# Kernel optimization log

Hardware: AMD Instinct MI355X
Metric: run time of the kernel (lower is better)

## Reference

```python
import jax, jax.numpy as jnp
import numpy as np

N_NODES = 100000
N_EDGES = 300000
D = 256
N_LAYERS = 4
BN_EPS = 1e-5


def setup_inputs() -> dict:
    key = jax.random.key(0)
    ks = jax.random.split(key, 6)
    x = jax.random.normal(ks[0], (N_NODES, D), dtype=jnp.float32)
    rows = jax.random.randint(ks[1], (N_EDGES,), 0, N_NODES)
    cols = jax.random.randint(ks[2], (N_EDGES,), 0, N_NODES)
    vals = jax.random.uniform(ks[3], (N_EDGES,), dtype=jnp.float32)
    stdv = 1.0 / np.sqrt(D).astype(np.float32)
    weights = jax.random.uniform(ks[4], (N_LAYERS, D, D), jnp.float32, -stdv, stdv)
    self_weights = jax.random.uniform(ks[5], (N_LAYERS, D, D), jnp.float32, -stdv, stdv)
    gammas = jnp.ones((N_LAYERS, D), jnp.float32)
    betas = jnp.zeros((N_LAYERS, D), jnp.float32)
    return {"x": x, "vals": vals, "weights": weights, "self_weights": self_weights,
            "gammas": gammas, "betas": betas, "rows": rows, "cols": cols}


def reference(x, vals, weights, self_weights, gammas, betas, rows, cols):
    n = x.shape[0]

    def gcn_layer(h, W, SW, gamma, beta):
        # support = h @ W  -> dense [N, D]
        support = h @ W
        # spmm(adj, support): out[i] = sum_{e: rows[e]==i} vals[e] * support[cols[e]]
        agg = jax.ops.segment_sum(vals[:, None] * support[cols], rows, num_segments=n)
        out = agg + h @ SW  # self-loop term (withloop=True)
        # BatchNorm1d over nodes (training-mode batch stats, biased variance)
        mean = out.mean(axis=0)
        var = out.var(axis=0)
        out = gamma * (out - mean) * jax.lax.rsqrt(var + BN_EPS) + beta
        return jax.nn.relu(out)

    h = x
    for i in range(N_LAYERS):
        h = gcn_layer(h, weights[i], self_weights[i], gammas[i], betas[i])
    # aggrmethod='concat', dense=False -> cat(final, input)
    return jnp.concatenate([h, x], axis=1)
```

## Files before the change

### kernel.cpp

```cpp
#include <hip/hip_runtime.h>
#include <hip/hip_bf16.h>
#include <stdint.h>

#define M_NODES 100000
#define NE      300000
#define D       256
#define D2      512
#define NLAYERS 4

#define SPMM_CHUNK 16

typedef float  f32x4  __attribute__((ext_vector_type(4)));
typedef __bf16 bf16x8 __attribute__((ext_vector_type(8)));

static __device__ __forceinline__ float bf2f(uint32_t u) {
  union { uint32_t i; float f; } v; v.i = u << 16; return v.f;
}
static __device__ __forceinline__ uint32_t f2bf(float f) {
  union { float f; uint32_t i; } v; v.f = f;
  return (v.i + 0x7fffu + ((v.i >> 16) & 1u)) >> 16;
}
static __device__ __forceinline__ void gload_lds16(const void* g, void* l) {
  __builtin_amdgcn_global_load_lds((const __attribute__((address_space(1))) uint32_t*)g,
                                   (__attribute__((address_space(3))) uint32_t*)l, 16, 0, 0);
}

__global__ void hist_kernel(const int* __restrict__ rows, int* __restrict__ counts) {
  int e = blockIdx.x * 256 + threadIdx.x;
  if (e < NE) atomicAdd(&counts[rows[e]], 1);
}

__global__ void scan1_kernel(const int* __restrict__ counts, int* __restrict__ rp,
                             int* __restrict__ bsum) {
  __shared__ int sd[256];
  int tid = threadIdx.x;
  int base = blockIdx.x * 1024 + tid * 4;
  int v0 = (base + 0 < M_NODES) ? counts[base + 0] : 0;
  int v1 = (base + 1 < M_NODES) ? counts[base + 1] : 0;
  int v2 = (base + 2 < M_NODES) ? counts[base + 2] : 0;
  int v3 = (base + 3 < M_NODES) ? counts[base + 3] : 0;
  int tsum = v0 + v1 + v2 + v3;
  sd[tid] = tsum; __syncthreads();
  for (int off = 1; off < 256; off <<= 1) {
    int x = sd[tid];
    if (tid >= off) x += sd[tid - off];
    __syncthreads(); sd[tid] = x; __syncthreads();
  }
  int excl = sd[tid] - tsum;
  if (base + 0 < M_NODES) rp[base + 0] = excl; excl += v0;
  if (base + 1 < M_NODES) rp[base + 1] = excl; excl += v1;
  if (base + 2 < M_NODES) rp[base + 2] = excl; excl += v2;
  if (base + 3 < M_NODES) rp[base + 3] = excl;
  if (tid == 255) bsum[blockIdx.x] = sd[255];
}

__global__ void scan2_kernel(const int* __restrict__ bsum, int* __restrict__ boff) {
  __shared__ int sd[128];
  int tid = threadIdx.x;
  int v = (tid < 98) ? bsum[tid] : 0;
  sd[tid] = v; __syncthreads();
  for (int off = 1; off < 128; off <<= 1) {
    int x = sd[tid];
    if (tid >= off) x += sd[tid - off];
    __syncthreads(); sd[tid] = x; __syncthreads();
  }
  if (tid < 98) boff[tid] = sd[tid] - v;
}

__global__ void scan3_kernel(int* __restrict__ rp, const int* __restrict__ boff,
                             int* __restrict__ cursor) {
  int i = blockIdx.x * 256 + threadIdx.x;
  if (i > M_NODES) return;
  int v = (i < M_NODES) ? rp[i] + boff[i >> 10] : NE;
  rp[i] = v;
  if (i < M_NODES) cursor[i] = v;
}

__global__ void scatter_kernel(const int* __restrict__ rows, const int* __restrict__ cols,
                               const float* __restrict__ vals, int* __restrict__ cursor,
                               uint2* __restrict__ emeta) {
  int e = blockIdx.x * 256 + threadIdx.x;
  if (e >= NE) return;
  int r = rows[e];
  int p = atomicAdd(&cursor[r], 1);
  uint2 m; m.x = (uint32_t)cols[e]; m.y = __float_as_uint(vals[e]);
  emeta[p] = m;
}

__global__ void prep_x_kernel(const float* __restrict__ x, float* __restrict__ out) {
  size_t idx = (size_t)blockIdx.x * 256 + threadIdx.x;
  size_t i = idx >> 6; int c = (int)(idx & 63) * 4;
  float4 v = *(const float4*)(x + i * D + c);
  *(float4*)(out + i * D2 + D + c) = v;
}

__global__ void conv_w_kernel(const float* __restrict__ W, const float* __restrict__ SW,
                              ushort* __restrict__ Bt) {
  int idx = blockIdx.x * 256 + threadIdx.x;
  if (idx >= NLAYERS * D2 * D) return;
  int k = idx & (D - 1);
  int n = (idx >> 8) & (D2 - 1);
  int layer = idx >> 17;
  float v = (n < D) ? W[(size_t)layer * D * D + k * D + n]
                    : SW[(size_t)layer * D * D + k * D + (n - D)];
  Bt[idx] = (ushort)f2bf(v);
}

__global__ void bn_fin_kernel(const float* __restrict__ stats, const float* __restrict__ gamma,
                              const float* __restrict__ beta, float* __restrict__ ss) {
  int c = threadIdx.x;
  float mean = stats[c] * (1.0f / M_NODES);
  float var  = stats[D + c] * (1.0f / M_NODES) - mean * mean;
  float rstd = rsqrtf(var + 1e-5f);
  float sc = gamma[c] * rstd;
  ss[c] = sc;
  ss[D + c] = beta[c] - mean * sc;
}

#define BM 128
#define BN 128
#define BK 64

template<int MODE>
__global__ __launch_bounds__(256, 2)
void gemm_kernel(const float* __restrict__ x, const ushort* __restrict__ P,
                 const float* __restrict__ ss, const ushort* __restrict__ Bt,
                 ushort* __restrict__ outAB) {
  __shared__ __align__(16) ushort As[BM * BK];
  __shared__ __align__(16) ushort Bs[BN * BK];
  const int tid = threadIdx.x;
  const int m0 = blockIdx.x * BM;
  const int n0 = blockIdx.y * BN;
  const int wv = tid >> 6, l = tid & 63;
  const int wr = wv >> 1, wc = wv & 1;
  const int lrow = l & 15, lhi = l >> 4;

  f32x4 acc[4][4] = {};

  const int arow = tid >> 3;
  const int acb  = (tid & 7) << 4;
  const int acol = acb >> 1;

#pragma unroll
  for (int s = 0; s < 4; ++s) {
    const int k0 = s * BK;
    float4 sc0, sc1, sh0, sh1;
    if (MODE == 1) {
      sc0 = *(const float4*)(ss + k0 + acol);
      sc1 = *(const float4*)(ss + k0 + acol + 4);
      sh0 = *(const float4*)(ss + D + k0 + acol);
      sh1 = *(const float4*)(ss + D + k0 + acol + 4);
    }
#pragma unroll
    for (int p = 0; p < 4; ++p) {
      int row = p * 32 + arow;
      int grow = m0 + row; if (grow >= M_NODES) grow = M_NODES - 1;
      float f[8];
      if (MODE == 0) {
        float4 v0 = *(const float4*)(x + (size_t)grow * D + k0 + acol);
        float4 v1 = *(const float4*)(x + (size_t)grow * D + k0 + acol + 4);
        f[0] = v0.x; f[1] = v0.y; f[2] = v0.z; f[3] = v0.w;
        f[4] = v1.x; f[5] = v1.y; f[6] = v1.z; f[7] = v1.w;
      } else {
        uint4 u = *(const uint4*)(P + (size_t)grow * D + k0 + acol);
        f[0] = fmaxf(bf2f(u.x & 0xffff) * sc0.x + sh0.x, 0.f);
        f[1] = fmaxf(bf2f(u.x >> 16)    * sc0.y + sh0.y, 0.f);
        f[2] = fmaxf(bf2f(u.y & 0xffff) * sc0.z + sh0.z, 0.f);
        f[3] = fmaxf(bf2f(u.y >> 16)    * sc0.w + sh0.w, 0.f);
        f[4] = fmaxf(bf2f(u.z & 0xffff) * sc1.x + sh1.x, 0.f);
        f[5] = fmaxf(bf2f(u.z >> 16)    * sc1.y + sh1.y, 0.f);
        f[6] = fmaxf(bf2f(u.w & 0xffff) * sc1.z + sh1.z, 0.f);
        f[7] = fmaxf(bf2f(u.w >> 16)    * sc1.w + sh1.w, 0.f);
      }
      uint4 o;
      o.x = f2bf(f[0]) | (f2bf(f[1]) << 16);
      o.y = f2bf(f[2]) | (f2bf(f[3]) << 16);
      o.z = f2bf(f[4]) | (f2bf(f[5]) << 16);
      o.w = f2bf(f[6]) | (f2bf(f[7]) << 16);
      *(uint4*)((char*)As + row * 128 + (acb ^ ((row & 7) << 4))) = o;
    }
#pragma unroll
    for (int p = 0; p < 4; ++p) {
      int row = p * 32 + arow;
      int gn = n0 + row;
      int gcb = acb ^ ((row & 7) << 4);
      gload_lds16(Bt + (size_t)gn * D + k0 + (gcb >> 1), Bs + row * BK + (acb >> 1));
    }
    __syncthreads();
#pragma unroll
    for (int kk = 0; kk < 2; ++kk) {
      bf16x8 af[4], bfr[4];
#pragma unroll
      for (int mi = 0; mi < 4; ++mi) {
        int row = wr * 64 + mi * 16 + lrow;
        int off = row * 128 + ((kk * 64 + lhi * 16) ^ ((row & 7) << 4));
        af[mi] = *(const bf16x8*)((const char*)As + off);
      }
#pragma unroll
      for (int nj = 0; nj < 4; ++nj) {
        int row = wc * 64 + nj * 16 + lrow;
        int off = row * 128 + ((kk * 64 + lhi * 16) ^ ((row & 7) << 4));
        bfr[nj] = *(const bf16x8*)((const char*)Bs + off);
      }
#pragma unroll
      for (int mi = 0; mi < 4; ++mi)
#pragma unroll
        for (int nj = 0; nj < 4; ++nj)
          acc[mi][nj] = __builtin_amdgcn_mfma_f32_16x16x32_bf16(af[mi], bfr[nj], acc[mi][nj], 0, 0, 0);
    }
    __syncthreads();
  }

#pragma unroll
  for (int mi = 0; mi < 4; ++mi) {
#pragma unroll
    for (int nj = 0; nj < 4; ++nj) {
      int gc = n0 + wc * 64 + nj * 16 + lrow;
#pragma unroll
      for (int r = 0; r < 4; ++r) {
        int grow = m0 + wr * 64 + mi * 16 + lhi * 4 + r;
        if (grow < M_NODES)
          outAB[(size_t)grow * D2 + gc] = (ushort)f2bf(acc[mi][nj][r]);
      }
    }
  }
}

__global__ __launch_bounds__(256, 8)
void spmm_kernel(const ushort* __restrict__ AB, ushort* __restrict__ P,
                 const int* __restrict__ rp, const uint2* __restrict__ emeta,
                 float* __restrict__ stats) {
  __shared__ float sstats[2 * D];
  for (int i = threadIdx.x; i < 2 * D; i += 256) sstats[i] = 0.f;
  __syncthreads();

  const int wv = threadIdx.x >> 6, l = threadIdx.x & 63;
  const int wave = blockIdx.x * 4 + wv;
  const int row0 = wave * SPMM_CHUNK;

  float s0 = 0, s1 = 0, s2 = 0, s3 = 0, q0 = 0, q1 = 0, q2 = 0, q3 = 0;

  if (row0 < M_NODES) {
    const int nrows = (M_NODES - row0 < SPMM_CHUNK) ? (M_NODES - row0) : SPMM_CHUNK;
    int myrp = (l <= nrows) ? rp[row0 + l] : 0;
    const int ebase = __shfl(myrp, 0);
    const int ecnt  = __shfl(myrp, nrows) - ebase;
    uint2 m0 = {0u, 0u}, m1 = {0u, 0u};
    if (l < ecnt)      m0 = emeta[ebase + l];
    if (64 + l < ecnt) m1 = emeta[ebase + 64 + l];

    for (int t = 0; t < nrows; ++t) {
      const int i = row0 + t;
      const int e0 = __shfl(myrp, t);
      const int e1 = __shfl(myrp, t + 1);
      const int deg = e1 - e0;

      const ushort4 st = *(const ushort4*)(AB + (size_t)i * D2 + D + 4 * l);
      float a0 = bf2f(st.x), a1 = bf2f(st.y), a2 = bf2f(st.z), a3 = bf2f(st.w);

      for (int b = 0; b < deg; b += 4) {
        float vv[4]; ushort4 sp[4];
#pragma unroll
        for (int j = 0; j < 4; ++j) {
          int ej = b + j;
          int ecl = (ej < deg) ? ej : (deg - 1);
          int slot = e0 - ebase + ecl;
          int sl = slot & 63;
          int cA = __shfl((int)m0.x, sl);
          int cB = __shfl((int)m1.x, sl);
          float vA = __shfl(__uint_as_float(m0.y), sl);
          float vB = __shfl(__uint_as_float(m1.y), sl);
          int   c = (slot < 64) ? cA : cB;
          float v = (slot < 64) ? vA : vB;
          if (slot >= 128 && ej < deg) {
            uint2 m = emeta[e0 + ecl]; c = (int)m.x; v = __uint_as_float(m.y);
          }
          vv[j] = (ej < deg) ? v : 0.f;
          sp[j] = *(const ushort4*)(AB + (size_t)c * D2 + 4 * l);
        }
#pragma unroll
        for (int j = 0; j < 4; ++j) {
          a0 += vv[j] * bf2f(sp[j].x); a1 += vv[j] * bf2f(sp[j].y);
          a2 += vv[j] * bf2f(sp[j].z); a3 += vv[j] * bf2f(sp[j].w);
        }
      }

      ushort4 o;
      o.x = (ushort)f2bf(a0); o.y = (ushort)f2bf(a1);
      o.z = (ushort)f2bf(a2); o.w = (ushort)f2bf(a3);
      *(ushort4*)(P + (size_t)i * D + 4 * l) = o;
      s0 += a0; q0 += a0 * a0; s1 += a1; q1 += a1 * a1;
      s2 += a2; q2 += a2 * a2; s3 += a3; q3 += a3 * a3;
    }
  }

  const int c0 = 4 * l;
  atomicAdd(&sstats[c0 + 0], s0); atomicAdd(&sstats[c0 + 1], s1);
  atomicAdd(&sstats[c0 + 2], s2); atomicAdd(&sstats[c0 + 3], s3);
  atomicAdd(&sstats[D + c0 + 0], q0); atomicAdd(&sstats[D + c0 + 1], q1);
  atomicAdd(&sstats[D + c0 + 2], q2); atomicAdd(&sstats[D + c0 + 3], q3);
  __syncthreads();
  atomicAdd(&stats[threadIdx.x], sstats[threadIdx.x]);
  atomicAdd(&stats[D + threadIdx.x], sstats[D + threadIdx.x]);
}

__global__ void norm_last_kernel(const ushort* __restrict__ P, const float* __restrict__ stats,
                                 const float* __restrict__ gamma, const float* __restrict__ beta,
                                 float* __restrict__ out) {
  const int cs = threadIdx.x & 31;
  const int rr = threadIdx.x >> 5;
  const int c0 = cs * 8;

  float sc[8], sh[8];
#pragma unroll
  for (int k = 0; k < 8; ++k) {
    float mean = stats[c0 + k] * (1.0f / M_NODES);
    float var  = stats[D + c0 + k] * (1.0f / M_NODES) - mean * mean;
    float rstd = rsqrtf(var + 1e-5f);
    float g = gamma[c0 + k];
    sc[k] = g * rstd;
    sh[k] = beta[c0 + k] - mean * sc[k];
  }

  const int r0 = blockIdx.x * 64;
#pragma unroll
  for (int rb = 0; rb < 8; ++rb) {
    int r = r0 + rb * 8 + rr;
    if (r >= M_NODES) break;
    const uint4 u = *(const uint4*)(P + (size_t)r * D + c0);
    float f[8];
    f[0] = bf2f(u.x & 0xffff); f[1] = bf2f(u.x >> 16);
    f[2] = bf2f(u.y & 0xffff); f[3] = bf2f(u.y >> 16);
    f[4] = bf2f(u.z & 0xffff); f[5] = bf2f(u.z >> 16);
    f[6] = bf2f(u.w & 0xffff); f[7] = bf2f(u.w >> 16);
#pragma unroll
    for (int k = 0; k < 8; ++k) f[k] = fmaxf(f[k] * sc[k] + sh[k], 0.f);
    float4 r0v = { f[0], f[1], f[2], f[3] };
    float4 r1v = { f[4], f[5], f[6], f[7] };
    *(float4*)(out + (size_t)r * D2 + c0) = r0v;
    *(float4*)(out + (size_t)r * D2 + c0 + 4) = r1v;
  }
}

extern "C" void kernel_launch(void* const* d_in, const int* in_sizes, int n_in,
                              void* d_out, int out_size, void* d_ws, size_t ws_size,
                              hipStream_t stream) {
  const float* x      = (const float*)d_in[0];
  const float* vals   = (const float*)d_in[1];
  const float* W      = (const float*)d_in[2];
  const float* SW     = (const float*)d_in[3];
  const float* gammas = (const float*)d_in[4];
  const float* betas  = (const float*)d_in[5];
  const int*   rows   = (const int*)d_in[6];
  const int*   cols   = (const int*)d_in[7];
  float* out = (float*)d_out;

  char* ws = (char*)d_ws;
  size_t off = 0;
  auto alloc = [&](size_t bytes) {
    void* p = ws + off;
    off = (off + bytes + 255) & ~(size_t)255;
    return p;
  };
  ushort* AB     = (ushort*)alloc((size_t)M_NODES * D2 * 2);
  ushort* P      = (ushort*)alloc((size_t)M_NODES * D * 2);
  ushort* Bt     = (ushort*)alloc((size_t)NLAYERS * D2 * D * 2);
  int*    rp     = (int*)alloc((M_NODES + 1) * 4);
  int*    cursor = (int*)alloc((M_NODES + 1) * 4);
  uint2*  emeta  = (uint2*)alloc((size_t)NE * 8);
  int*    bsum   = (int*)alloc(512);
  int*    boff   = (int*)alloc(512);
  float*  stats  = (float*)alloc(NLAYERS * 2 * D * 4);
  float*  ss     = (float*)alloc(2 * D * 4);

  hipMemsetAsync(cursor, 0, (size_t)M_NODES * 4, stream);
  hipMemsetAsync(stats, 0, (size_t)NLAYERS * 2 * D * 4, stream);

  hist_kernel<<<(NE + 255) / 256, 256, 0, stream>>>(rows, cursor);
  scan1_kernel<<<98, 256, 0, stream>>>(cursor, rp, bsum);
  scan2_kernel<<<1, 128, 0, stream>>>(bsum, boff);
  scan3_kernel<<<(M_NODES + 256) / 256, 256, 0, stream>>>(rp, boff, cursor);
  scatter_kernel<<<(NE + 255) / 256, 256, 0, stream>>>(rows, cols, vals, cursor, emeta);

  prep_x_kernel<<<(M_NODES * D / 4) / 256, 256, 0, stream>>>(x, out);
  conv_w_kernel<<<(NLAYERS * D2 * D) / 256, 256, 0, stream>>>(W, SW, Bt);

  const dim3 ggrid((M_NODES + BM - 1) / BM, D2 / BN);
  const int spmm_blocks = (M_NODES + SPMM_CHUNK * 4 - 1) / (SPMM_CHUNK * 4);
  for (int lyr = 0; lyr < NLAYERS; ++lyr) {
    if (lyr == 0)
      gemm_kernel<0><<<ggrid, 256, 0, stream>>>(x, nullptr, nullptr,
                                                Bt + (size_t)lyr * D2 * D, AB);
    else
      gemm_kernel<1><<<ggrid, 256, 0, stream>>>(nullptr, P, ss,
                                                Bt + (size_t)lyr * D2 * D, AB);
    spmm_kernel<<<spmm_blocks, 256, 0, stream>>>(AB, P, rp, emeta,
                                                 stats + (size_t)lyr * 2 * D);
    if (lyr < NLAYERS - 1)
      bn_fin_kernel<<<1, 256, 0, stream>>>(stats + (size_t)lyr * 2 * D,
                                           gammas + lyr * D, betas + lyr * D, ss);
    else
      norm_last_kernel<<<(M_NODES + 63) / 64, 256, 0, stream>>>(
          P, stats + (size_t)lyr * 2 * D, gammas + lyr * D, betas + lyr * D, out);
  }
}
```

Before: 712.0 us.

## Fuse BN finalize and x copy into GEMM, stage output through LDS

Removes the separate prep_x and bn_fin kernels. The x copy into the output is folded into the first-layer GEMM (done by blockIdx.x==0 blocks), and the BN scale/shift is computed inline from the raw stats inside the GEMM A-load. The grid is transposed so the N tiles of the same M rows run adjacently, which should improve reuse of A rows in L2. The GEMM epilogue now stages results in LDS so it can write coalesced 16-byte rows instead of scattered 2-byte stores. In exchange, every GEMM thread redoes the rsqrt and stats loads, and the epilogue adds an extra LDS pass plus a barrier.

```diff
diff --git a/kernel.cpp b/kernel.cpp
--- a/kernel.cpp
+++ b/kernel.cpp
@@ -87,13 +87,6 @@
   emeta[p] = m;
 }
 
-__global__ void prep_x_kernel(const float* __restrict__ x, float* __restrict__ out) {
-  size_t idx = (size_t)blockIdx.x * 256 + threadIdx.x;
-  size_t i = idx >> 6; int c = (int)(idx & 63) * 4;
-  float4 v = *(const float4*)(x + i * D + c);
-  *(float4*)(out + i * D2 + D + c) = v;
-}
-
 __global__ void conv_w_kernel(const float* __restrict__ W, const float* __restrict__ SW,
                               ushort* __restrict__ Bt) {
   int idx = blockIdx.x * 256 + threadIdx.x;
@@ -106,17 +99,6 @@
   Bt[idx] = (ushort)f2bf(v);
 }
 
-__global__ void bn_fin_kernel(const float* __restrict__ stats, const float* __restrict__ gamma,
-                              const float* __restrict__ beta, float* __restrict__ ss) {
-  int c = threadIdx.x;
-  float mean = stats[c] * (1.0f / M_NODES);
-  float var  = stats[D + c] * (1.0f / M_NODES) - mean * mean;
-  float rstd = rsqrtf(var + 1e-5f);
-  float sc = gamma[c] * rstd;
-  ss[c] = sc;
-  ss[D + c] = beta[c] - mean * sc;
-}
-
 #define BM 128
 #define BN 128
 #define BK 64
@@ -124,13 +106,15 @@
 template<int MODE>
 __global__ __launch_bounds__(256, 2)
 void gemm_kernel(const float* __restrict__ x, const ushort* __restrict__ P,
-                 const float* __restrict__ ss, const ushort* __restrict__ Bt,
-                 ushort* __restrict__ outAB) {
-  __shared__ __align__(16) ushort As[BM * BK];
-  __shared__ __align__(16) ushort Bs[BN * BK];
+                 const float* __restrict__ stats, const float* __restrict__ gamma,
+                 const float* __restrict__ beta, const ushort* __restrict__ Bt,
+                 ushort* __restrict__ outAB, float* __restrict__ out) {
+  __shared__ __align__(16) ushort smem[BM * BK + BN * BK];
+  ushort* As = smem;
+  ushort* Bs = smem + BM * BK;
   const int tid = threadIdx.x;
-  const int m0 = blockIdx.x * BM;
-  const int n0 = blockIdx.y * BN;
+  const int n0 = blockIdx.x * BN;
+  const int m0 = blockIdx.y * BM;
   const int wv = tid >> 6, l = tid & 63;
   const int wr = wv >> 1, wc = wv & 1;
   const int lrow = l & 15, lhi = l >> 4;
@@ -144,33 +128,52 @@
 #pragma unroll
   for (int s = 0; s < 4; ++s) {
     const int k0 = s * BK;
-    float4 sc0, sc1, sh0, sh1;
+    float sc[8], sh[8];
     if (MODE == 1) {
-      sc0 = *(const float4*)(ss + k0 + acol);
-      sc1 = *(const float4*)(ss + k0 + acol + 4);
-      sh0 = *(const float4*)(ss + D + k0 + acol);
-      sh1 = *(const float4*)(ss + D + k0 + acol + 4);
+      float sm[8], sq[8], gg[8], bb[8];
+      *(float4*)(sm)     = *(const float4*)(stats + k0 + acol);
+      *(float4*)(sm + 4) = *(const float4*)(stats + k0 + acol + 4);
+      *(float4*)(sq)     = *(const float4*)(stats + D + k0 + acol);
+      *(float4*)(sq + 4) = *(const float4*)(stats + D + k0 + acol + 4);
+      *(float4*)(gg)     = *(const float4*)(gamma + k0 + acol);
+      *(float4*)(gg + 4) = *(const float4*)(gamma + k0 + acol + 4);
+      *(float4*)(bb)     = *(const float4*)(beta + k0 + acol);
+      *(float4*)(bb + 4) = *(const float4*)(beta + k0 + acol + 4);
+#pragma unroll
+      for (int k = 0; k < 8; ++k) {
+        float mean = sm[k] * (1.0f / M_NODES);
+        float var  = sq[k] * (1.0f / M_NODES) - mean * mean;
+        float rstd = rsqrtf(var + 1e-5f);
+        sc[k] = gg[k] * rstd;
+        sh[k] = bb[k] - mean * sc[k];
+      }
     }
 #pragma unroll
     for (int p = 0; p < 4; ++p) {
       int row = p * 32 + arow;
-      int grow = m0 + row; if (grow >= M_NODES) grow = M_NODES - 1;
+      int grow = m0 + row;
+      const bool inb = grow < M_NODES;
+      if (!inb) grow = M_NODES - 1;
       float f[8];
       if (MODE == 0) {
         float4 v0 = *(const float4*)(x + (size_t)grow * D + k0 + acol);
         float4 v1 = *(const float4*)(x + (size_t)grow * D + k0 + acol + 4);
         f[0] = v0.x; f[1] = v0.y; f[2] = v0.z; f[3] = v0.w;
         f[4] = v1.x; f[5] = v1.y; f[6] = v1.z; f[7] = v1.w;
+        if (blockIdx.x == 0 && inb) {
+          *(float4*)(out + (size_t)grow * D2 + D + k0 + acol) = v0;
+          *(float4*)(out + (size_t)grow * D2 + D + k0 + acol + 4) = v1;
+        }
       } else {
         uint4 u = *(const uint4*)(P + (size_t)grow * D + k0 + acol);
-        f[0] = fmaxf(bf2f(u.x & 0xffff) * sc0.x + sh0.x, 0.f);
-        f[1] = fmaxf(bf2f(u.x >> 16)    * sc0.y + sh0.y, 0.f);
-        f[2] = fmaxf(bf2f(u.y & 0xffff) * sc0.z + sh0.z, 0.f);
-        f[3] = fmaxf(bf2f(u.y >> 16)    * sc0.w + sh0.w, 0.f);
-        f[4] = fmaxf(bf2f(u.z & 0xffff) * sc1.x + sh1.x, 0.f);
-        f[5] = fmaxf(bf2f(u.z >> 16)    * sc1.y + sh1.y, 0.f);
-        f[6] = fmaxf(bf2f(u.w & 0xffff) * sc1.z + sh1.z, 0.f);
-        f[7] = fmaxf(bf2f(u.w >> 16)    * sc1.w + sh1.w, 0.f);
+        f[0] = fmaxf(bf2f(u.x & 0xffff) * sc[0] + sh[0], 0.f);
+        f[1] = fmaxf(bf2f(u.x >> 16)    * sc[1] + sh[1], 0.f);
+        f[2] = fmaxf(bf2f(u.y & 0xffff) * sc[2] + sh[2], 0.f);
+        f[3] = fmaxf(bf2f(u.y >> 16)    * sc[3] + sh[3], 0.f);
+        f[4] = fmaxf(bf2f(u.z & 0xffff) * sc[4] + sh[4], 0.f);
+        f[5] = fmaxf(bf2f(u.z >> 16)    * sc[5] + sh[5], 0.f);
+        f[6] = fmaxf(bf2f(u.w & 0xffff) * sc[6] + sh[6], 0.f);
+        f[7] = fmaxf(bf2f(u.w >> 16)    * sc[7] + sh[7], 0.f);
       }
       uint4 o;
       o.x = f2bf(f[0]) | (f2bf(f[1]) << 16);
@@ -212,16 +215,24 @@
   }
 
 #pragma unroll
-  for (int mi = 0; mi < 4; ++mi) {
-#pragma unroll
-    for (int nj = 0; nj < 4; ++nj) {
-      int gc = n0 + wc * 64 + nj * 16 + lrow;
+  for (int mi = 0; mi < 4; ++mi)
+#pragma unroll
+    for (int nj = 0; nj < 4; ++nj)
 #pragma unroll
       for (int r = 0; r < 4; ++r) {
-        int grow = m0 + wr * 64 + mi * 16 + lhi * 4 + r;
-        if (grow < M_NODES)
-          outAB[(size_t)grow * D2 + gc] = (ushort)f2bf(acc[mi][nj][r]);
-      }
+        int rl = wr * 64 + mi * 16 + lhi * 4 + r;
+        int cl = wc * 64 + nj * 16 + lrow;
+        smem[rl * 128 + (cl ^ ((rl & 7) << 3))] = (ushort)f2bf(acc[mi][nj][r]);
+      }
+  __syncthreads();
+  const int rg = tid >> 4, lc16 = tid & 15;
+#pragma unroll
+  for (int i = 0; i < 8; ++i) {
+    int rl = i * 16 + rg;
+    int grow = m0 + rl;
+    if (grow < M_NODES) {
+      uint4 v = *(const uint4*)(smem + rl * 128 + ((lc16 * 8) ^ ((rl & 7) << 3)));
+      *(uint4*)(outAB + (size_t)grow * D2 + n0 + lc16 * 8) = v;
     }
   }
 }
@@ -371,7 +382,6 @@
   int*    bsum   = (int*)alloc(512);
   int*    boff   = (int*)alloc(512);
   float*  stats  = (float*)alloc(NLAYERS * 2 * D * 4);
-  float*  ss     = (float*)alloc(2 * D * 4);
 
   hipMemsetAsync(cursor, 0, (size_t)M_NODES * 4, stream);
   hipMemsetAsync(stats, 0, (size_t)NLAYERS * 2 * D * 4, stream);
@@ -382,25 +392,23 @@
   scan3_kernel<<<(M_NODES + 256) / 256, 256, 0, stream>>>(rp, boff, cursor);
   scatter_kernel<<<(NE + 255) / 256, 256, 0, stream>>>(rows, cols, vals, cursor, emeta);
 
-  prep_x_kernel<<<(M_NODES * D / 4) / 256, 256, 0, stream>>>(x, out);
   conv_w_kernel<<<(NLAYERS * D2 * D) / 256, 256, 0, stream>>>(W, SW, Bt);
 
-  const dim3 ggrid((M_NODES + BM - 1) / BM, D2 / BN);
+  const dim3 ggrid(D2 / BN, (M_NODES + BM - 1) / BM);
   const int spmm_blocks = (M_NODES + SPMM_CHUNK * 4 - 1) / (SPMM_CHUNK * 4);
   for (int lyr = 0; lyr < NLAYERS; ++lyr) {
     if (lyr == 0)
-      gemm_kernel<0><<<ggrid, 256, 0, stream>>>(x, nullptr, nullptr,
-                                                Bt + (size_t)lyr * D2 * D, AB);
+      gemm_kernel<0><<<ggrid, 256, 0, stream>>>(x, nullptr, nullptr, nullptr, nullptr,
+                                                Bt + (size_t)lyr * D2 * D, AB, out);
     else
-      gemm_kernel<1><<<ggrid, 256, 0, stream>>>(nullptr, P, ss,
-                                                Bt + (size_t)lyr * D2 * D, AB);
+      gemm_kernel<1><<<ggrid, 256, 0, stream>>>(nullptr, P, stats + (size_t)(lyr - 1) * 2 * D,
+                                                gammas + (size_t)(lyr - 1) * D,
+                                                betas + (size_t)(lyr - 1) * D,
+                                                Bt + (size_t)lyr * D2 * D, AB, nullptr);
     spmm_kernel<<<spmm_blocks, 256, 0, stream>>>(AB, P, rp, emeta,
                                                  stats + (size_t)lyr * 2 * D);
-    if (lyr < NLAYERS - 1)
-      bn_fin_kernel<<<1, 256, 0, stream>>>(stats + (size_t)lyr * 2 * D,
-                                           gammas + lyr * D, betas + lyr * D, ss);
-    else
-      norm_last_kernel<<<(M_NODES + 63) / 64, 256, 0, stream>>>(
-          P, stats + (size_t)lyr * 2 * D, gammas + lyr * D, betas + lyr * D, out);
-  }
-}
+  }
+  norm_last_kernel<<<(M_NODES + 63) / 64, 256, 0, stream>>>(
+      P, stats + (size_t)(NLAYERS - 1) * 2 * D, gammas + (size_t)(NLAYERS - 1) * D,
+      betas + (size_t)(NLAYERS - 1) * D, out);
+}
```

Measured after the change: 748.5 us. 1.05x slower.
